# Performance work log

Hardware: AMD Instinct MI355X
Metric: run time of the kernel (lower is better)

## Reference

```python
import jax, jax.numpy as jnp
import numpy as np

NUM_HEADS = 8
OUT_FEATURES = 64
ALPHA = 0.2


def setup_inputs() -> dict:
    key = jax.random.key(0)
    k1, k2, k3, k4 = jax.random.split(key, 4)
    B, N, E, F_IN = 2, 8192, 4096, 256
    x = jax.random.normal(k1, (B, N, F_IN), dtype=jnp.float32)
    H = jax.random.uniform(k2, (N, E), dtype=jnp.float32)
    # xavier-like scaled params
    W = jax.random.normal(k3, (F_IN, OUT_FEATURES * NUM_HEADS), dtype=jnp.float32) * 0.05
    a_vertices = jax.random.normal(k4, (OUT_FEATURES, 1), dtype=jnp.float32) * 0.1
    return {"x": x, "H": H, "W": W, "a_vertices": a_vertices}


def reference(x, H, W, a_vertices):
    B, N, _ = x.shape
    # Wh: (B, N, heads, out)
    Wh = jnp.matmul(x, W).reshape(B, N, NUM_HEADS, OUT_FEATURES)
    # per-node, per-head attention logit: (B, N, heads)
    av = jax.nn.leaky_relu(jnp.einsum('bnhd,d->bnh', Wh, a_vertices[:, 0]), ALPHA)
    # edge attention: softmax over edges (torch dim=0 of (E, heads))
    ae = jax.nn.softmax(jnp.einsum('ne,bnh->beh', H, av), axis=1)  # (B, E, heads)
    # aggregate node features onto edges: (B, E, heads, out)
    m = jnp.einsum('ne,bnhd->behd', H, Wh)
    # scatter back to nodes with edge-attention weighting: (B, N, heads, out)
    out = jnp.einsum('ne,beh,behd->bnhd', H, ae, m)
    return out.reshape(B, N, NUM_HEADS * OUT_FEATURES)
```

## Files before the change

### kernel.cpp

```cpp
#include <hip/hip_runtime.h>

#define N_NODES 8192
#define N_EDGES 4096
#define F_INS   256
#define HEADS   8
#define DOUT    64
#define HDIM    512
#define CCOMB   1024
#define BATCH   2

typedef __bf16 bf16x8 __attribute__((ext_vector_type(8)));
typedef __bf16 bf16x4 __attribute__((ext_vector_type(4)));
typedef float  f32x4  __attribute__((ext_vector_type(4)));

__device__ __forceinline__ void gld_lds16(const __bf16* g, __bf16* l) {
    __builtin_amdgcn_global_load_lds(
        (const __attribute__((address_space(1))) void*)g,
        (__attribute__((address_space(3))) void*)l, 16, 0, 0);
}

__launch_bounds__(256)
__global__ void convert_H_logits_kernel(const float* __restrict__ H,
                                        const float* __restrict__ av,
                                        __bf16* __restrict__ Hb,
                                        __bf16* __restrict__ HbT,
                                        float* __restrict__ logits) {
    __shared__ float lav[512 * 16];
    __shared__ __bf16 tile[32][33];
    __shared__ float red[256 * 16];
    int t = threadIdx.x;
    int e0 = blockIdx.x * 32;
    int n0 = blockIdx.y * 512;
    for (int p = t; p < 8192; p += 256) {
        int b = p >> 12, rem = p & 4095, i = rem >> 3, h = rem & 7;
        lav[i * 16 + b * 8 + h] = av[(size_t)b * (N_NODES * 8) + (size_t)(n0 + i) * 8 + h];
    }
    __syncthreads();
    int c = t & 31, r0 = t >> 5;
    float acc[16];
#pragma unroll
    for (int q = 0; q < 16; ++q) acc[q] = 0.f;
    for (int sub = 0; sub < 16; ++sub) {
        int nb = n0 + sub * 32;
#pragma unroll
        for (int p = 0; p < 4; ++p) {
            int r = p * 8 + r0;
            float v = H[(size_t)(nb + r) * N_EDGES + e0 + c];
            __bf16 bv = (__bf16)v;
            Hb[(size_t)(nb + r) * N_EDGES + e0 + c] = bv;
            tile[r][c] = bv;
            const float* lr = &lav[(sub * 32 + r) * 16];
#pragma unroll
            for (int q = 0; q < 16; ++q) acc[q] += v * lr[q];
        }
        __syncthreads();
#pragma unroll
        for (int p = 0; p < 4; ++p) {
            int er = p * 8 + r0;
            HbT[(size_t)(e0 + er) * N_NODES + nb + c] = tile[c][er];
        }
        __syncthreads();
    }
#pragma unroll
    for (int q = 0; q < 16; ++q) red[t * 16 + q] = acc[q];
    __syncthreads();
    for (int o = t; o < 512; o += 256) {
        int e = o & 31, q = o >> 5;
        float s = 0.f;
#pragma unroll
        for (int r8 = 0; r8 < 8; ++r8) s += red[(r8 * 32 + e) * 16 + q];
        atomicAdd(&logits[(size_t)q * N_EDGES + e0 + e], s);
    }
}

__launch_bounds__(256)
__global__ void wbt_kernel(const float* __restrict__ W, __bf16* __restrict__ WbT) {
    int i = blockIdx.x * 256 + threadIdx.x;
    int c = i >> 8, f = i & 255;
    WbT[i] = (__bf16)W[(size_t)f * HDIM + c];
}

__launch_bounds__(256)
__global__ void wa_kernel(const float* __restrict__ W, const float* __restrict__ a,
                          float* __restrict__ Wa) {
    int i = blockIdx.x * 256 + threadIdx.x;
    if (i >= F_INS * HEADS) return;
    int f = i >> 3, h = i & 7;
    float s = 0.f;
#pragma unroll 8
    for (int d = 0; d < DOUT; ++d) s += W[(size_t)f * HDIM + h * DOUT + d] * a[d];
    Wa[i] = s;
}

__launch_bounds__(256)
__global__ void av_kernel(const float* __restrict__ x, const float* __restrict__ Wa,
                          float* __restrict__ av, __bf16* __restrict__ xb) {
    __shared__ float lx[32][257];
    __shared__ float lwa[F_INS * HEADS];
    int t = threadIdx.x;
    size_t row0 = (size_t)blockIdx.x * 32;
    for (int p = t; p < F_INS * HEADS; p += 256) lwa[p] = Wa[p];
#pragma unroll
    for (int p = 0; p < 32; ++p) {
        float v = x[(row0 + p) * F_INS + t];
        lx[p][t] = v;
        xb[(row0 + p) * F_INS + t] = (__bf16)v;
    }
    __syncthreads();
    int r = t >> 3, h = t & 7;
    float acc = 0.f;
#pragma unroll 8
    for (int f = 0; f < F_INS; ++f) acc += lx[r][f] * lwa[f * 8 + h];
    av[(row0 + r) * 8 + h] = acc > 0.f ? acc : 0.2f * acc;
}

__launch_bounds__(256)
__global__ void softmax_kernel(float* __restrict__ logits) {
    __shared__ float red[4];
    __shared__ float reds[4];
    int t = threadIdx.x;
    float* row = logits + (size_t)blockIdx.x * N_EDGES;
    float mx = -1e30f;
    for (int i = t; i < N_EDGES; i += 256) mx = fmaxf(mx, row[i]);
#pragma unroll
    for (int o = 32; o > 0; o >>= 1) mx = fmaxf(mx, __shfl_xor(mx, o, 64));
    if ((t & 63) == 0) red[t >> 6] = mx;
    __syncthreads();
    mx = fmaxf(fmaxf(red[0], red[1]), fmaxf(red[2], red[3]));
    float s = 0.f;
    for (int i = t; i < N_EDGES; i += 256) {
        float v = expf(row[i] - mx);
        row[i] = v;
        s += v;
    }
#pragma unroll
    for (int o = 32; o > 0; o >>= 1) s += __shfl_xor(s, o, 64);
    if ((t & 63) == 0) reds[t >> 6] = s;
    __syncthreads();
    float inv = 1.0f / (reds[0] + reds[1] + reds[2] + reds[3]);
    for (int i = t; i < N_EDGES; i += 256) row[i] *= inv;
}

template <int MODE>
__launch_bounds__(256, 4)
__global__ void gemm_bt(const __bf16* __restrict__ A, const __bf16* __restrict__ BT,
                        int lda, int ldbt, int K,
                        size_t a_bz, size_t bt_bz, size_t out_z,
                        __bf16* __restrict__ outB, int ldo,
                        float* __restrict__ outF) {
    __shared__ __bf16 AsF[8192];
    __shared__ __bf16 BsF[8192];
    int t = threadIdx.x;
    int bz = blockIdx.z;
    A  += (size_t)bz * a_bz;
    BT += (size_t)bz * bt_bz;
    if (MODE == 0) outB += (size_t)bz * out_z;
    if (MODE == 1) outF += (size_t)bz * out_z;
    size_t m0 = (size_t)blockIdx.y * 128;
    size_t n0 = (size_t)blockIdx.x * 128;

    int lane = t & 63, wv = t >> 6;
    int ln = lane & 15, lk = lane >> 4;

    const __bf16* pA[4]; const __bf16* pB[4];
    __bf16* lA[4]; __bf16* lB[4];
#pragma unroll
    for (int p = 0; p < 4; ++p) {
        int bid = wv * 4 + p;
        int mb = bid >> 1, kb = bid & 1;
        pA[p] = A + (m0 + mb * 16 + ln) * (size_t)lda + kb * 32 + lk * 8;
        pB[p] = BT + (n0 + mb * 16 + ln) * (size_t)ldbt + kb * 32 + lk * 8;
        lA[p] = &AsF[bid * 512];
        lB[p] = &BsF[bid * 512];
    }

    int wm16 = (wv & 1) * 4, wn16 = (wv >> 1) * 4;
    f32x4 acc[4][4] = {};

    for (int k0 = 0; k0 < K; k0 += 64) {
        __syncthreads();
#pragma unroll
        for (int p = 0; p < 4; ++p) gld_lds16(pA[p] + k0, lA[p]);
#pragma unroll
        for (int p = 0; p < 4; ++p) gld_lds16(pB[p] + k0, lB[p]);
        __syncthreads();
#pragma unroll
        for (int ksb = 0; ksb < 2; ++ksb) {
            bf16x8 af[4], bfr[4];
#pragma unroll
            for (int i = 0; i < 4; ++i)
                af[i] = *(const bf16x8*)&AsF[((wm16 + i) * 2 + ksb) * 512 + lane * 8];
#pragma unroll
            for (int j = 0; j < 4; ++j)
                bfr[j] = *(const bf16x8*)&BsF[((wn16 + j) * 2 + ksb) * 512 + lane * 8];
#pragma unroll
            for (int i = 0; i < 4; ++i)
#pragma unroll
                for (int j = 0; j < 4; ++j)
                    acc[i][j] = __builtin_amdgcn_mfma_f32_16x16x32_bf16(
                        af[i], bfr[j], acc[i][j], 0, 0, 0);
        }
    }

    int wm = (wv & 1) * 64, wn = (wv >> 1) * 64;
#pragma unroll
    for (int i = 0; i < 4; ++i)
#pragma unroll
        for (int j = 0; j < 4; ++j)
#pragma unroll
            for (int rg = 0; rg < 4; ++rg) {
                int gm = (int)m0 + wm + i * 16 + lk * 4 + rg;
                int gc = (int)n0 + wn + j * 16 + ln;
                float v = acc[i][j][rg];
                if (MODE == 0) {
                    outB[(size_t)gm * ldo + gc] = (__bf16)v;
                } else if (MODE == 1) {
                    outF[(size_t)gm * ldo + gc] = v;
                } else {
                    outF[(size_t)(gc >> 9) * ((size_t)N_NODES * HDIM) +
                         (size_t)gm * HDIM + (gc & 511)] = v;
                }
            }
}

__launch_bounds__(256)
__global__ void scale1_kernel(const float* __restrict__ acc1, const float* __restrict__ ae,
                              __bf16* __restrict__ mwT) {
    int i = blockIdx.x * 256 + threadIdx.x;
    size_t base = (size_t)i * 4;
    int c = (int)(base >> 12);
    int e = (int)(base & 4095);
    const size_t slab = (size_t)CCOMB * N_EDGES / 4;
    float4 s0 = ((const float4*)acc1)[i];
    float4 s1 = ((const float4*)acc1)[i + slab];
    float4 s2 = ((const float4*)acc1)[i + 2 * slab];
    float4 s3 = ((const float4*)acc1)[i + 3 * slab];
    float4 a4 = *(const float4*)(ae + ((size_t)(c >> 6) << 12) + e);
    bf16x4 o;
    o.x = (__bf16)((s0.x + s1.x + s2.x + s3.x) * a4.x);
    o.y = (__bf16)((s0.y + s1.y + s2.y + s3.y) * a4.y);
    o.z = (__bf16)((s0.z + s1.z + s2.z + s3.z) * a4.z);
    o.w = (__bf16)((s0.w + s1.w + s2.w + s3.w) * a4.w);
    ((bf16x4*)mwT)[i] = o;
}

extern "C" void kernel_launch(void* const* d_in, const int* in_sizes, int n_in,
                              void* d_out, int out_size, void* d_ws, size_t ws_size,
                              hipStream_t stream) {
    const float* x = (const float*)d_in[0];
    const float* H = (const float*)d_in[1];
    const float* W = (const float*)d_in[2];
    const float* a = (const float*)d_in[3];
    float* out = (float*)d_out;

    char* p = (char*)d_ws;
    __bf16* Hb   = (__bf16*)p; p += (size_t)N_NODES * N_EDGES * 2;
    __bf16* HbT  = (__bf16*)p; p += (size_t)N_EDGES * N_NODES * 2;
    __bf16* xb   = (__bf16*)p; p += (size_t)BATCH * N_NODES * F_INS * 2;
    __bf16* WbT  = (__bf16*)p; p += (size_t)HDIM * F_INS * 2;
    __bf16* WhbT = (__bf16*)p; p += (size_t)CCOMB * N_NODES * 2;
    __bf16* mwT  = (__bf16*)p; p += (size_t)CCOMB * N_EDGES * 2;
    float*  Wa   = (float*)p;  p += (size_t)F_INS * HEADS * 4;
    float*  av   = (float*)p;  p += (size_t)BATCH * N_NODES * HEADS * 4;
    float*  ae   = (float*)p;  p += (size_t)16 * N_EDGES * 4;
    float*  acc1 = (float*)p;  p += (size_t)4 * CCOMB * N_EDGES * 4;

    hipMemsetAsync(ae, 0, (size_t)16 * N_EDGES * 4, stream);

    wbt_kernel<<<dim3(HDIM * F_INS / 256), 256, 0, stream>>>(W, WbT);
    wa_kernel<<<dim3(8), 256, 0, stream>>>(W, a, Wa);
    av_kernel<<<dim3(BATCH * N_NODES / 32), 256, 0, stream>>>(x, Wa, av, xb);
    convert_H_logits_kernel<<<dim3(N_EDGES / 32, N_NODES / 512), 256, 0, stream>>>(
        H, av, Hb, HbT, ae);
    softmax_kernel<<<dim3(16), 256, 0, stream>>>(ae);

    gemm_bt<0><<<dim3(64, 4, 2), 256, 0, stream>>>(
        WbT, xb, F_INS, F_INS, F_INS,
        0, (size_t)N_NODES * F_INS, (size_t)HDIM * N_NODES,
        WhbT, N_NODES, nullptr);

    gemm_bt<1><<<dim3(32, 8, 4), 256, 0, stream>>>(
        WhbT, HbT, N_NODES, N_NODES, 2048,
        2048, 2048, (size_t)CCOMB * N_EDGES,
        nullptr, N_EDGES, acc1);

    scale1_kernel<<<dim3(CCOMB * N_EDGES / 4 / 256), 256, 0, stream>>>(acc1, ae, mwT);

    gemm_bt<2><<<dim3(8, 64, 1), 256, 0, stream>>>(
        Hb, mwT, N_EDGES, N_EDGES, N_EDGES,
        0, 0, 0,
        nullptr, 0, out);
}
```

Baseline: 567.4 us.

## Use 256x256-tile 512-thread GEMM with split-K and XCD swizzle for big matmuls

Adds a new 256x256 tiled bf16 MFMA GEMM kernel with 512 threads, a 4-stage global-to-LDS pipeline and an optional XCD-aware block remap. It replaces the two large GEMMs (edge aggregation and node scatter). The final GEMM now uses split-K over two halves, writing partial sums to a workspace that a new reduce kernel adds and permutes into the output layout. Larger tiles raise data reuse and MFMA density, at the cost of an extra fp32 partial-sum round trip and fewer blocks per launch.

```diff
diff --git a/kernel.cpp b/kernel.cpp
--- a/kernel.cpp
+++ b/kernel.cpp
@@ -220,6 +220,109 @@
                     outF[(size_t)(gc >> 9) * ((size_t)N_NODES * HDIM) +
                          (size_t)gm * HDIM + (gc & 511)] = v;
                 }
+            }
+}
+
+template <int SWZ>
+__launch_bounds__(512, 2)
+__global__ void gemm256(const __bf16* __restrict__ A, const __bf16* __restrict__ BT,
+                        int lda, int ldbt, int K,
+                        size_t a_bz, size_t bt_bz, size_t out_z,
+                        float* __restrict__ outF, int ldo) {
+    __shared__ __bf16 lds[4 * 32 * 512];
+    int bx, by, bz;
+    if (SWZ) {
+        int g = (int)blockIdx.x + 4 * ((int)blockIdx.y + 32 * (int)blockIdx.z);
+        int xcd = g & 7, j = g >> 3;
+        int l = (j & 3) + 4 * xcd + 32 * (j >> 2);
+        bx = l & 3; by = (l >> 2) & 31; bz = l >> 7;
+    } else {
+        bx = blockIdx.x; by = blockIdx.y; bz = blockIdx.z;
+    }
+    A    += (size_t)bz * a_bz;
+    BT   += (size_t)bz * bt_bz;
+    outF += (size_t)bz * out_z;
+    size_t m0 = (size_t)by * 256;
+    size_t n0 = (size_t)bx * 256;
+
+    int t = threadIdx.x;
+    int lane = t & 63, wv = t >> 6;
+    int ln = lane & 15, lk = lane >> 4;
+
+    int fw = wv * 2;
+    const __bf16* gA0 = A + (m0 + fw * 16 + ln) * (size_t)lda + lk * 8;
+    const __bf16* gA1 = gA0 + 16 * (size_t)lda;
+    const __bf16* gB0 = BT + (n0 + fw * 16 + ln) * (size_t)ldbt + lk * 8;
+    const __bf16* gB1 = gB0 + 16 * (size_t)ldbt;
+
+    int NT = K >> 5;
+
+    for (int tt = 0; tt < 3; ++tt) {
+        __bf16* d = &lds[tt * 16384];
+        gld_lds16(gA0 + tt * 32, d + fw * 512);
+        gld_lds16(gA1 + tt * 32, d + (fw + 1) * 512);
+        gld_lds16(gB0 + tt * 32, d + (16 + fw) * 512);
+        gld_lds16(gB1 + tt * 32, d + (16 + fw + 1) * 512);
+    }
+    asm volatile("s_waitcnt vmcnt(8)" ::: "memory");
+    __builtin_amdgcn_s_barrier();
+    __builtin_amdgcn_sched_barrier(0);
+
+    f32x4 acc[8][4] = {};
+    int wmf = (wv >> 2) * 8;
+    int wnf = (wv & 3) * 4;
+
+    auto compute = [&](int tl) {
+        const __bf16* buf = &lds[(tl & 3) * 16384];
+        bf16x8 af[8], bfr[4];
+#pragma unroll
+        for (int i = 0; i < 8; ++i)
+            af[i] = *(const bf16x8*)(buf + (wmf + i) * 512 + lane * 8);
+#pragma unroll
+        for (int j = 0; j < 4; ++j)
+            bfr[j] = *(const bf16x8*)(buf + (16 + wnf + j) * 512 + lane * 8);
+        __builtin_amdgcn_s_setprio(1);
+#pragma unroll
+        for (int i = 0; i < 8; ++i)
+#pragma unroll
+            for (int j = 0; j < 4; ++j)
+                acc[i][j] = __builtin_amdgcn_mfma_f32_16x16x32_bf16(
+                    af[i], bfr[j], acc[i][j], 0, 0, 0);
+        __builtin_amdgcn_s_setprio(0);
+    };
+
+    for (int tl = 0; tl < NT - 3; ++tl) {
+        __bf16* d = &lds[((tl + 3) & 3) * 16384];
+        int off = (tl + 3) * 32;
+        gld_lds16(gA0 + off, d + fw * 512);
+        gld_lds16(gA1 + off, d + (fw + 1) * 512);
+        gld_lds16(gB0 + off, d + (16 + fw) * 512);
+        gld_lds16(gB1 + off, d + (16 + fw + 1) * 512);
+        compute(tl);
+        asm volatile("s_waitcnt vmcnt(8)" ::: "memory");
+        __builtin_amdgcn_s_barrier();
+        __builtin_amdgcn_sched_barrier(0);
+    }
+    compute(NT - 3);
+    asm volatile("s_waitcnt vmcnt(4)" ::: "memory");
+    __builtin_amdgcn_s_barrier();
+    __builtin_amdgcn_sched_barrier(0);
+    compute(NT - 2);
+    asm volatile("s_waitcnt vmcnt(0)" ::: "memory");
+    __builtin_amdgcn_s_barrier();
+    __builtin_amdgcn_sched_barrier(0);
+    compute(NT - 1);
+
+    int wm = (wv >> 2) * 128, wn = (wv & 3) * 64;
+#pragma unroll
+    for (int i = 0; i < 8; ++i)
+#pragma unroll
+        for (int j = 0; j < 4; ++j)
+#pragma unroll
+            for (int rg = 0; rg < 4; ++rg) {
+                int gm = (int)m0 + wm + i * 16 + lk * 4 + rg;
+                int gc = (int)n0 + wn + j * 16 + ln;
+                outF[(size_t)gm * ldo + gc] = acc[i][j][rg];
             }
 }
 
@@ -244,6 +347,21 @@
     ((bf16x4*)mwT)[i] = o;
 }
 
+__launch_bounds__(256)
+__global__ void reduce2_kernel(const float* __restrict__ s, float* __restrict__ out) {
+    int i = blockIdx.x * 256 + threadIdx.x;
+    size_t base = (size_t)i * 4;
+    int m = (int)(base >> 10);
+    int c = (int)(base & 1023);
+    const size_t slab = (size_t)N_NODES * CCOMB / 4;
+    float4 a = ((const float4*)s)[i];
+    float4 b = ((const float4*)s)[i + slab];
+    float4 o;
+    o.x = a.x + b.x; o.y = a.y + b.y; o.z = a.z + b.z; o.w = a.w + b.w;
+    *(float4*)&out[(size_t)(c >> 9) * ((size_t)N_NODES * HDIM) +
+                   (size_t)m * HDIM + (c & 511)] = o;
+}
+
 extern "C" void kernel_launch(void* const* d_in, const int* in_sizes, int n_in,
                               void* d_out, int out_size, void* d_ws, size_t ws_size,
                               hipStream_t stream) {
@@ -279,15 +397,17 @@
         0, (size_t)N_NODES * F_INS, (size_t)HDIM * N_NODES,
         WhbT, N_NODES, nullptr);
 
-    gemm_bt<1><<<dim3(32, 8, 4), 256, 0, stream>>>(
+    gemm256<0><<<dim3(16, 4, 4), 512, 0, stream>>>(
         WhbT, HbT, N_NODES, N_NODES, 2048,
         2048, 2048, (size_t)CCOMB * N_EDGES,
-        nullptr, N_EDGES, acc1);
+        acc1, N_EDGES);
 
     scale1_kernel<<<dim3(CCOMB * N_EDGES / 4 / 256), 256, 0, stream>>>(acc1, ae, mwT);
 
-    gemm_bt<2><<<dim3(8, 64, 1), 256, 0, stream>>>(
-        Hb, mwT, N_EDGES, N_EDGES, N_EDGES,
-        0, 0, 0,
-        nullptr, 0, out);
-}
+    gemm256<1><<<dim3(4, 32, 2), 512, 0, stream>>>(
+        Hb, mwT, N_EDGES, N_EDGES, 2048,
+        2048, 2048, (size_t)N_NODES * CCOMB,
+        acc1, CCOMB);
+
+    reduce2_kernel<<<dim3(N_NODES * CCOMB / 4 / 256), 256, 0, stream>>>(acc1, out);
+}
```

New measurement: 485.7 us. 14.4% less time.
